# Kernel tuning notes

Measured on AMD Instinct MI355X. Metric: run time of the kernel, lower is better.

## Reference

```python
import jax, jax.numpy as jnp
import numpy as np

HEADS, D_K = 8, 64   # dim=512 -> d_k = dim//heads = 64; with dim_head=64 the rearrange collapses to [B,H,N,d_k]
EPS = 1e-5


def _per_head_layernorm(t, g, b):
    # t: [B,H,N,D]; g,b: [H,D] (independent LayerNorm per head, biased variance like torch)
    mu = t.mean(-1, keepdims=True)
    var = ((t - mu) ** 2).mean(-1, keepdims=True)
    return (t - mu) * jax.lax.rsqrt(var + EPS) * g[None, :, None, :] + b[None, :, None, :]


def setup_inputs() -> dict:
    key = jax.random.key(0)
    k0, k1, k2, k3, k4, k5 = jax.random.split(key, 6)
    B, N, DIM = 4, 2048, 512
    inner = HEADS * D_K  # = DIM here
    x = jax.random.normal(k0, (B, N, DIM), jnp.float32)
    W_qkv = jax.random.normal(k1, (DIM, 3 * inner), jnp.float32) * (DIM ** -0.5)  # xavier-ish, no bias
    g_q = 1.0 + 0.1 * jax.random.normal(k2, (HEADS, D_K), jnp.float32)
    b_q = 0.1 * jax.random.normal(k3, (HEADS, D_K), jnp.float32)
    g_k = 1.0 + 0.1 * jax.random.normal(k4, (HEADS, D_K), jnp.float32)
    b_k = 0.1 * jax.random.normal(k5, (HEADS, D_K), jnp.float32)
    return {"x": x, "W_qkv": W_qkv, "g_q": g_q, "b_q": b_q, "g_k": g_k, "b_k": b_k}


def reference(x, W_qkv, g_q, b_q, g_k, b_k):
    B, N, _ = x.shape
    qkv = x @ W_qkv                              # [B,N,3*H*D]
    q, k, v = jnp.split(qkv, 3, axis=-1)

    def split_heads(t):
        return t.reshape(B, N, HEADS, D_K).transpose(0, 2, 1, 3)  # [B,H,N,D]

    q, k, v = map(split_heads, (q, k, v))
    q = _per_head_layernorm(q, g_q, b_q)
    k = _per_head_layernorm(k, g_k, b_k)
    # un-normalized linear attention: scale by 1/sqrt(d_k) then by 1/seq_len (no softmax)
    dots = jnp.einsum('bhnd,bhmd->bhnm', q, k) * (D_K ** -0.5)
    p_attn = dots / N
    out = jnp.einsum('bhnm,bhmd->bhnd', p_attn, v)  # [B,H,N,D]
    return out.transpose(0, 2, 1, 3).reshape(B, N, HEADS * D_K)
```

## Files before the change

### kernel.cpp

```cpp
#include <hip/hip_runtime.h>
#include <hip/hip_bf16.h>
#include <stdint.h>

using bf16   = __bf16;
using bf16x4 = __attribute__((ext_vector_type(4))) __bf16;
using bf16x8 = __attribute__((ext_vector_type(8))) __bf16;
using f32x4  = __attribute__((ext_vector_type(4))) float;

static constexpr int BATCH = 4, SEQ = 2048, DIM = 512, HEADS = 8, DK = 64;
static constexpr int M    = BATCH * SEQ;
static constexpr int NQKV = 3 * DIM;

#define GLD16(src, dst)                                                        \
    __builtin_amdgcn_global_load_lds(                                          \
        (const __attribute__((address_space(1))) void*)(src),                  \
        (__attribute__((address_space(3))) void*)(dst), 16, 0, 0)

__global__ __launch_bounds__(256) void k_prep(const float* __restrict__ w,
                                              bf16* __restrict__ wt)
{
    const int bid = blockIdx.x;
    const int t   = threadIdx.x;
    const int rt = bid / 48, ct = bid - rt * 48;
    __shared__ float tile[32][33];
    const int r = t >> 5, c = t & 31;
    #pragma unroll
    for (int i = 0; i < 4; ++i)
        tile[r + i * 8][c] = w[(rt * 32 + r + i * 8) * NQKV + ct * 32 + c];
    __syncthreads();
    #pragma unroll
    for (int i = 0; i < 4; ++i)
        wt[(ct * 32 + r + i * 8) * DIM + rt * 32 + c] = (bf16)tile[c][r + i * 8];
}

__global__ __launch_bounds__(384) void k_gemm(const float* __restrict__ x,
                                              const bf16* __restrict__ Wt,
                                              const float* __restrict__ gq,
                                              const float* __restrict__ bq,
                                              const float* __restrict__ gk,
                                              const float* __restrict__ bk,
                                              bf16* __restrict__ qn,
                                              float* __restrict__ Sp)
{
    __shared__ union {
        struct { bf16 A[128 * 64]; bf16 B[192 * 64]; } g;
        struct { bf16 q[2][64][72]; bf16 kst[64 * 128]; bf16 vst[64 * 128]; } e;
    } u;

    const int t    = threadIdx.x;
    const int lane = t & 63, wave = t >> 6;
    const int wm   = wave & 1, ws = wave >> 1;
    const int orig = blockIdx.x;
    const int wg   = (orig & 7) * 64 + (orig >> 3);
    const int mt   = wg >> 3, h = wg & 7;
    const int m0   = mt * 128;

    const int l15 = lane & 15, l4 = lane >> 4;
    const int rl  = lane >> 3, cl = (lane & 7) ^ rl;

    f32x4 acc[4][4] = {};

    for (int k0 = 0; k0 < 512; k0 += 64) {
        #pragma unroll
        for (int i = 0; i < 4; ++i) {
            const int ch  = wave * 4 + i;
            const int sec = ch >> 3;
            const int r   = (ch & 7) * 8 + rl;
            GLD16(Wt + ((sec * 512 + h * 64 + r) * 512 + k0 + cl * 8),
                  u.g.B + ch * 512);
        }
        for (int i = t; i < 2048; i += 384) {
            const int row = i >> 4, ch = i & 15;
            float4 v = *(const float4*)(x + (m0 + row) * 512 + k0 + ch * 4);
            bf16x4 o = { (bf16)v.x, (bf16)v.y, (bf16)v.z, (bf16)v.w };
            *(bf16x4*)(u.g.A + row * 64 + (((ch >> 1) ^ (row & 7)) * 8) + (ch & 1) * 4) = o;
        }
        __syncthreads();
        #pragma unroll
        for (int kh = 0; kh < 2; ++kh) {
            bf16x8 af[4], bfv[4];
            const int rc = kh * 4 + l4;
            #pragma unroll
            for (int mf = 0; mf < 4; ++mf) {
                const int row = wm * 64 + mf * 16 + l15;
                af[mf] = *(const bf16x8*)(u.g.A + row * 64 + ((rc ^ (row & 7)) * 8));
            }
            #pragma unroll
            for (int nf = 0; nf < 4; ++nf) {
                const int row = ws * 64 + nf * 16 + l15;
                bfv[nf] = *(const bf16x8*)(u.g.B + row * 64 + ((rc ^ (row & 7)) * 8));
            }
            #pragma unroll
            for (int mf = 0; mf < 4; ++mf)
                #pragma unroll
                for (int nf = 0; nf < 4; ++nf)
                    acc[mf][nf] = __builtin_amdgcn_mfma_f32_16x16x32_bf16(
                        af[mf], bfv[nf], acc[mf][nf], 0, 0, 0);
        }
        __syncthreads();
    }

    const int b  = m0 >> 11;
    const int bh = b * 8 + h;
    const int nwbase = (m0 & 2047) + wm * 64;

    if (ws < 2) {
        const float* gp = (ws == 0 ? gq : gk) + h * 64;
        const float* bp = (ws == 0 ? bq : bk) + h * 64;
        float gv[4], bv[4];
        #pragma unroll
        for (int nf = 0; nf < 4; ++nf) {
            gv[nf] = gp[nf * 16 + l15];
            bv[nf] = bp[nf * 16 + l15];
        }
        #pragma unroll
        for (int mf = 0; mf < 4; ++mf) {
            float mu[4], rs[4];
            #pragma unroll
            for (int r = 0; r < 4; ++r) {
                float s = 0.f, s2 = 0.f;
                #pragma unroll
                for (int nf = 0; nf < 4; ++nf) {
                    const float xv = acc[mf][nf][r];
                    s += xv; s2 += xv * xv;
                }
                s  += __shfl_xor(s, 1);  s  += __shfl_xor(s, 2);
                s  += __shfl_xor(s, 4);  s  += __shfl_xor(s, 8);
                s2 += __shfl_xor(s2, 1); s2 += __shfl_xor(s2, 2);
                s2 += __shfl_xor(s2, 4); s2 += __shfl_xor(s2, 8);
                mu[r] = s * (1.f / 64.f);
                rs[r] = rsqrtf(s2 * (1.f / 64.f) - mu[r] * mu[r] + 1e-5f);
            }
            #pragma unroll
            for (int nf = 0; nf < 4; ++nf) {
                bf16x4 pk;
                #pragma unroll
                for (int r = 0; r < 4; ++r)
                    pk[r] = (bf16)((acc[mf][nf][r] - mu[r]) * rs[r] * gv[nf] + bv[nf]);
                if (ws == 0) {
                    *(bf16x4*)(&u.e.q[wm][nf * 16 + l15][mf * 16 + l4 * 4]) = pk;
                } else {
                    const int d = nf * 16 + l15;
                    const int c = wm * 8 + mf * 2 + (l4 >> 1);
                    *(bf16x4*)(u.e.kst + d * 128 + ((c ^ (d & 7)) * 8) + (l4 & 1) * 4) = pk;
                }
            }
        }
    } else {
        #pragma unroll
        for (int mf = 0; mf < 4; ++mf)
            #pragma unroll
            for (int nf = 0; nf < 4; ++nf) {
                bf16x4 pk;
                #pragma unroll
                for (int r = 0; r < 4; ++r) pk[r] = (bf16)acc[mf][nf][r];
                const int d = nf * 16 + l15;
                const int c = wm * 8 + mf * 2 + (l4 >> 1);
                *(bf16x4*)(u.e.vst + d * 128 + ((c ^ (d & 7)) * 8) + (l4 & 1) * 4) = pk;
            }
    }

    if (ws == 0) {
        bf16* dst = qn + ((long)bh * SEQ + nwbase) * 64;
        const int nq = lane & 15, dq2 = lane >> 4;
        #pragma unroll
        for (int j = 0; j < 4; ++j) {
            const int d0 = (j * 4 + dq2) * 4;
            bf16x4 a0 = *(const bf16x4*)(&u.e.q[wm][d0 + 0][nq * 4]);
            bf16x4 a1 = *(const bf16x4*)(&u.e.q[wm][d0 + 1][nq * 4]);
            bf16x4 a2 = *(const bf16x4*)(&u.e.q[wm][d0 + 2][nq * 4]);
            bf16x4 a3 = *(const bf16x4*)(&u.e.q[wm][d0 + 3][nq * 4]);
            #pragma unroll
            for (int c = 0; c < 4; ++c) {
                bf16x4 o = { a0[c], a1[c], a2[c], a3[c] };
                *(bf16x4*)(dst + (nq * 4 + c) * 64 + d0) = o;
            }
        }
    }

    __syncthreads();

    if (ws == 2) {
        f32x4 sac[4][4] = {};
        #pragma unroll
        for (int kk = 0; kk < 2; ++kk) {
            const int ksi = wm * 2 + kk;
            const int c   = ksi * 4 + l4;
            bf16x8 av[4], bk8[4];
            #pragma unroll
            for (int i = 0; i < 4; ++i) {
                const int dp = i * 16 + l15;
                av[i] = *(const bf16x8*)(u.e.vst + dp * 128 + ((c ^ (dp & 7)) * 8));
            }
            #pragma unroll
            for (int j = 0; j < 4; ++j) {
                const int dd = j * 16 + l15;
                bk8[j] = *(const bf16x8*)(u.e.kst + dd * 128 + ((c ^ (dd & 7)) * 8));
            }
            #pragma unroll
            for (int i = 0; i < 4; ++i)
                #pragma unroll
                for (int j = 0; j < 4; ++j)
                    sac[i][j] = __builtin_amdgcn_mfma_f32_16x16x32_bf16(
                        av[i], bk8[j], sac[i][j], 0, 0, 0);
        }
        float* red = (float*)u.e.q;
        if (wm == 0) {
            #pragma unroll
            for (int i = 0; i < 4; ++i)
                #pragma unroll
                for (int j = 0; j < 4; ++j)
                    *(f32x4*)(red + ((i * 16 + l4 * 4) * 64 + j * 16 + l15) + 0) =
                        (f32x4){0.f, 0.f, 0.f, 0.f};
        }
        if (wm == 0) {
            #pragma unroll
            for (int i = 0; i < 4; ++i)
                #pragma unroll
                for (int j = 0; j < 4; ++j)
                    #pragma unroll
                    for (int r = 0; r < 4; ++r)
                        red[(i * 16 + l4 * 4 + r) * 64 + j * 16 + l15] = sac[i][j][r];
        }
        __builtin_amdgcn_s_barrier();
        if (wm == 1) {
            float* Sb = Sp + (long)(mt * 8 + h) * 4096;
            #pragma unroll
            for (int i = 0; i < 4; ++i)
                #pragma unroll
                for (int j = 0; j < 4; ++j)
                    #pragma unroll
                    for (int r = 0; r < 4; ++r) {
                        const int dp = i * 16 + l4 * 4 + r;
                        const int dd = j * 16 + l15;
                        Sb[dp * 64 + dd] = sac[i][j][r] + red[dp * 64 + dd];
                    }
        }
    }
}

__global__ __launch_bounds__(256) void k_out(const bf16* __restrict__ qn,
                                             const float* __restrict__ Sp,
                                             float* __restrict__ out)
{
    __shared__ float sS[64 * 68];
    const int bid = blockIdx.x;
    const int bh = bid >> 3, nt8 = bid & 7;
    const int b = bh >> 3, h = bh & 7;
    const int t = threadIdx.x, lane = t & 63, wave = t >> 6;
    const int l15 = lane & 15, l4 = lane >> 4;

    f32x4 racc[4] = {};
    for (int mt16 = 0; mt16 < 16; ++mt16) {
        const float* p = Sp + (long)(((b * 16 + mt16) * 8) + h) * 4096 + t * 4;
        #pragma unroll
        for (int j = 0; j < 4; ++j)
            racc[j] += *(const f32x4*)(p + j * 1024);
    }
    #pragma unroll
    for (int j = 0; j < 4; ++j) {
        const int f  = j * 1024 + t * 4;
        const int dp = f >> 6, dd = f & 63;
        *(f32x4*)(sS + dp * 68 + dd) = racc[j];
    }
    __syncthreads();

    const float scale = 1.f / 16384.f;
    bf16x8 bfr[2][4];
    #pragma unroll
    for (int kh = 0; kh < 2; ++kh)
        #pragma unroll
        for (int cf = 0; cf < 4; ++cf) {
            const float* p = sS + (cf * 16 + l15) * 68 + kh * 32 + l4 * 8;
            float4 lo = *(const float4*)(p);
            float4 hi = *(const float4*)(p + 4);
            bf16x8 f;
            f[0] = (bf16)(lo.x * scale); f[1] = (bf16)(lo.y * scale);
            f[2] = (bf16)(lo.z * scale); f[3] = (bf16)(lo.w * scale);
            f[4] = (bf16)(hi.x * scale); f[5] = (bf16)(hi.y * scale);
            f[6] = (bf16)(hi.z * scale); f[7] = (bf16)(hi.w * scale);
            bfr[kh][cf] = f;
        }

    const bf16* qb = qn + (long)bh * SEQ * 64;
    const int nbase = nt8 * 256 + wave * 64;

    #pragma unroll
    for (int mf = 0; mf < 4; ++mf) {
        bf16x8 a0 = *(const bf16x8*)(qb + (nbase + mf * 16 + l15) * 64 +      l4 * 8);
        bf16x8 a1 = *(const bf16x8*)(qb + (nbase + mf * 16 + l15) * 64 + 32 + l4 * 8);
        f32x4 acc[4] = {};
        #pragma unroll
        for (int cf = 0; cf < 4; ++cf) {
            acc[cf] = __builtin_amdgcn_mfma_f32_16x16x32_bf16(a0, bfr[0][cf], acc[cf], 0, 0, 0);
            acc[cf] = __builtin_amdgcn_mfma_f32_16x16x32_bf16(a1, bfr[1][cf], acc[cf], 0, 0, 0);
        }
        #pragma unroll
        for (int cf = 0; cf < 4; ++cf)
            #pragma unroll
            for (int r = 0; r < 4; ++r) {
                const int n = nbase + mf * 16 + l4 * 4 + r;
                out[((long)b * SEQ + n) * 512 + h * 64 + cf * 16 + l15] = acc[cf][r];
            }
    }
}

extern "C" void kernel_launch(void* const* d_in, const int* in_sizes, int n_in,
                              void* d_out, int out_size, void* d_ws, size_t ws_size,
                              hipStream_t stream)
{
    const float* x  = (const float*)d_in[0];
    const float* w  = (const float*)d_in[1];
    const float* gq = (const float*)d_in[2];
    const float* bq = (const float*)d_in[3];
    const float* gk = (const float*)d_in[4];
    const float* bk = (const float*)d_in[5];
    float* out = (float*)d_out;

    char* ws = (char*)d_ws;
    bf16*  wt = (bf16*)(ws);
    bf16*  qn = (bf16*)(ws + 1572864);
    float* Sp = (float*)(ws + 9961472);

    hipLaunchKernelGGL(k_prep, dim3(768), dim3(256), 0, stream, w, wt);
    hipLaunchKernelGGL(k_gemm, dim3(512), dim3(384), 0, stream,
                       x, wt, gq, bq, gk, bk, qn, Sp);
    hipLaunchKernelGGL(k_out,  dim3(256), dim3(256), 0, stream, qn, Sp, out);
}
```

Baseline: 119.9 us.

## Double GEMM K-tile, add separate S-reduction kernel, and split output kernel finer

```diff
diff --git a/kernel.cpp b/kernel.cpp
--- a/kernel.cpp
+++ b/kernel.cpp
@@ -43,7 +43,7 @@
                                               float* __restrict__ Sp)
 {
     __shared__ union {
-        struct { bf16 A[128 * 64]; bf16 B[192 * 64]; } g;
+        struct { bf16 A[128 * 128]; bf16 B[192 * 128]; } g;
         struct { bf16 q[2][64][72]; bf16 kst[64 * 128]; bf16 vst[64 * 128]; } e;
     } u;
 
@@ -56,39 +56,46 @@
     const int m0   = mt * 128;
 
     const int l15 = lane & 15, l4 = lane >> 4;
-    const int rl  = lane >> 3, cl = (lane & 7) ^ rl;
+    const int rl  = lane >> 4;
+    const int clB = lane & 15;
 
     f32x4 acc[4][4] = {};
 
-    for (int k0 = 0; k0 < 512; k0 += 64) {
-        #pragma unroll
-        for (int i = 0; i < 4; ++i) {
-            const int ch  = wave * 4 + i;
-            const int sec = ch >> 3;
-            const int r   = (ch & 7) * 8 + rl;
-            GLD16(Wt + ((sec * 512 + h * 64 + r) * 512 + k0 + cl * 8),
+    for (int k0 = 0; k0 < 512; k0 += 128) {
+        #pragma unroll
+        for (int i = 0; i < 8; ++i) {
+            const int ch  = wave * 8 + i;
+            const int rL  = ch * 4 + rl;
+            const int sec = rL >> 6, rin = rL & 63;
+            GLD16(Wt + ((sec * 512 + h * 64 + rin) * 512 + k0
+                        + ((clB ^ (rL & 15)) * 8)),
                   u.g.B + ch * 512);
         }
-        for (int i = t; i < 2048; i += 384) {
-            const int row = i >> 4, ch = i & 15;
-            float4 v = *(const float4*)(x + (m0 + row) * 512 + k0 + ch * 4);
-            bf16x4 o = { (bf16)v.x, (bf16)v.y, (bf16)v.z, (bf16)v.w };
-            *(bf16x4*)(u.g.A + row * 64 + (((ch >> 1) ^ (row & 7)) * 8) + (ch & 1) * 4) = o;
+        #pragma unroll
+        for (int j = 0; j < 11; ++j) {
+            const int i = t + j * 384;
+            if (i < 4096) {
+                const int row = i >> 5, ch = i & 31;
+                float4 v = *(const float4*)(x + (long)(m0 + row) * 512 + k0 + ch * 4);
+                bf16x4 o = { (bf16)v.x, (bf16)v.y, (bf16)v.z, (bf16)v.w };
+                *(bf16x4*)(u.g.A + row * 128 + (((ch >> 1) ^ (row & 15)) * 8)
+                           + (ch & 1) * 4) = o;
+            }
         }
         __syncthreads();
         #pragma unroll
-        for (int kh = 0; kh < 2; ++kh) {
+        for (int kh = 0; kh < 4; ++kh) {
             bf16x8 af[4], bfv[4];
             const int rc = kh * 4 + l4;
             #pragma unroll
             for (int mf = 0; mf < 4; ++mf) {
                 const int row = wm * 64 + mf * 16 + l15;
-                af[mf] = *(const bf16x8*)(u.g.A + row * 64 + ((rc ^ (row & 7)) * 8));
+                af[mf] = *(const bf16x8*)(u.g.A + row * 128 + ((rc ^ (row & 15)) * 8));
             }
             #pragma unroll
             for (int nf = 0; nf < 4; ++nf) {
                 const int row = ws * 64 + nf * 16 + l15;
-                bfv[nf] = *(const bf16x8*)(u.g.B + row * 64 + ((rc ^ (row & 7)) * 8));
+                bfv[nf] = *(const bf16x8*)(u.g.B + row * 128 + ((rc ^ (row & 15)) * 8));
             }
             #pragma unroll
             for (int mf = 0; mf < 4; ++mf)
@@ -210,14 +217,6 @@
             for (int i = 0; i < 4; ++i)
                 #pragma unroll
                 for (int j = 0; j < 4; ++j)
-                    *(f32x4*)(red + ((i * 16 + l4 * 4) * 64 + j * 16 + l15) + 0) =
-                        (f32x4){0.f, 0.f, 0.f, 0.f};
-        }
-        if (wm == 0) {
-            #pragma unroll
-            for (int i = 0; i < 4; ++i)
-                #pragma unroll
-                for (int j = 0; j < 4; ++j)
                     #pragma unroll
                     for (int r = 0; r < 4; ++r)
                         red[(i * 16 + l4 * 4 + r) * 64 + j * 16 + l15] = sac[i][j][r];
@@ -239,29 +238,36 @@
     }
 }
 
+__global__ __launch_bounds__(256) void k_red(const float* __restrict__ Sp,
+                                             float* __restrict__ S)
+{
+    const int bid = blockIdx.x;
+    const int bh = bid >> 4, chunk = bid & 15;
+    const int b = bh >> 3, h = bh & 7;
+    const int e = chunk * 256 + threadIdx.x;
+    float s = 0.f;
+    #pragma unroll 4
+    for (int p = 0; p < 16; ++p)
+        s += Sp[((long)((b * 16 + p) * 8 + h)) * 4096 + e];
+    S[(long)bh * 4096 + e] = s;
+}
+
 __global__ __launch_bounds__(256) void k_out(const bf16* __restrict__ qn,
-                                             const float* __restrict__ Sp,
+                                             const float* __restrict__ S,
                                              float* __restrict__ out)
 {
     __shared__ float sS[64 * 68];
     const int bid = blockIdx.x;
-    const int bh = bid >> 3, nt8 = bid & 7;
+    const int bh = bid >> 4, nt16 = bid & 15;
     const int b = bh >> 3, h = bh & 7;
     const int t = threadIdx.x, lane = t & 63, wave = t >> 6;
     const int l15 = lane & 15, l4 = lane >> 4;
 
-    f32x4 racc[4] = {};
-    for (int mt16 = 0; mt16 < 16; ++mt16) {
-        const float* p = Sp + (long)(((b * 16 + mt16) * 8) + h) * 4096 + t * 4;
-        #pragma unroll
-        for (int j = 0; j < 4; ++j)
-            racc[j] += *(const f32x4*)(p + j * 1024);
-    }
     #pragma unroll
     for (int j = 0; j < 4; ++j) {
         const int f  = j * 1024 + t * 4;
         const int dp = f >> 6, dd = f & 63;
-        *(f32x4*)(sS + dp * 68 + dd) = racc[j];
+        *(f32x4*)(sS + dp * 68 + dd) = *(const f32x4*)(S + (long)bh * 4096 + f);
     }
     __syncthreads();
 
@@ -283,10 +289,10 @@
         }
 
     const bf16* qb = qn + (long)bh * SEQ * 64;
-    const int nbase = nt8 * 256 + wave * 64;
-
-    #pragma unroll
-    for (int mf = 0; mf < 4; ++mf) {
+    const int nbase = nt16 * 128 + wave * 32;
+
+    #pragma unroll
+    for (int mf = 0; mf < 2; ++mf) {
         bf16x8 a0 = *(const bf16x8*)(qb + (nbase + mf * 16 + l15) * 64 +      l4 * 8);
         bf16x8 a1 = *(const bf16x8*)(qb + (nbase + mf * 16 + l15) * 64 + 32 + l4 * 8);
         f32x4 acc[4] = {};
@@ -321,9 +327,11 @@
     bf16*  wt = (bf16*)(ws);
     bf16*  qn = (bf16*)(ws + 1572864);
     float* Sp = (float*)(ws + 9961472);
+    float* S  = (float*)(ws + 18350080);
 
     hipLaunchKernelGGL(k_prep, dim3(768), dim3(256), 0, stream, w, wt);
     hipLaunchKernelGGL(k_gemm, dim3(512), dim3(384), 0, stream,
                        x, wt, gq, bq, gk, bk, qn, Sp);
-    hipLaunchKernelGGL(k_out,  dim3(256), dim3(256), 0, stream, qn, Sp, out);
-}
+    hipLaunchKernelGGL(k_red,  dim3(512), dim3(256), 0, stream, Sp, S);
+    hipLaunchKernelGGL(k_out,  dim3(512), dim3(256), 0, stream, qn, S, out);
+}
```

Measured after the change: 131.1 us. 1.09x slower.
